# Optimization experiments

Measured on AMD Instinct MI355X. Metric: run time of the kernel, lower is better.

Reference implementation:

```python
import jax, jax.numpy as jnp
import numpy as np

NUM_HEADS = 4
LN_EPS = 1e-5


def _gcn_layer(src, dst, feats, skip_w, skip_b, msg_w, msg_b):
    # DGL GCNLayer: symmetric degree norm (from src rows), copy_u+sum aggregation,
    # msg linear + affine skip. No activation is applied in the original forward.
    n = feats.shape[0]
    deg = jax.ops.segment_sum(jnp.ones(src.shape, feats.dtype), src, num_segments=n)
    dinv = jnp.where(deg > 0, deg ** -0.5, jnp.zeros_like(deg))
    h = feats * dinv[:, None]                                  # [N, D]
    agg = jax.ops.segment_sum(h[src], dst, num_segments=n)     # scatter-sum over edges
    rst = agg * dinv[:, None]
    return rst @ msg_w.T + msg_b + feats @ skip_w.T + skip_b


def _layernorm(x, g, b):
    mu = jnp.mean(x, axis=-1, keepdims=True)
    var = jnp.mean((x - mu) ** 2, axis=-1, keepdims=True)
    return (x - mu) * jax.lax.rsqrt(var + LN_EPS) * g + b


def _cross_attention(x, seq, in_proj_w, in_proj_b, out_proj_w, out_proj_b, ln_g, ln_b):
    # Unbatched torch nn.MultiheadAttention(query=x [N,D], key=value=seq [S,D]).
    n, d = x.shape
    hd = d // NUM_HEADS
    wq, wk, wv = in_proj_w[:d], in_proj_w[d:2 * d], in_proj_w[2 * d:]
    bq, bk, bv = in_proj_b[:d], in_proj_b[d:2 * d], in_proj_b[2 * d:]
    q = (x @ wq.T + bq).reshape(n, NUM_HEADS, hd)
    k = (seq @ wk.T + bk).reshape(-1, NUM_HEADS, hd)
    v = (seq @ wv.T + bv).reshape(-1, NUM_HEADS, hd)
    scores = jnp.einsum('nhd,shd->hns', q, k) / jnp.sqrt(jnp.asarray(hd, x.dtype))
    attn = jax.nn.softmax(scores, axis=-1)
    o = jnp.einsum('hns,shd->nhd', attn, v).reshape(n, d)
    o = o @ out_proj_w.T + out_proj_b
    # dropout is identity in eval mode; residual + layernorm (num_cross_att == 1 path)
    return _layernorm(o + x, ln_g, ln_b)


def reference(x, seq_embeddings, src, dst, edge_label_index,
              skip_w0, skip_b0, msg_w0, msg_b0,
              skip_w1, skip_b1, msg_w1, msg_b1,
              in_proj_w, in_proj_b, out_proj_w, out_proj_b, ln_g, ln_b,
              weight1, weight2):
    x = _gcn_layer(src, dst, x, skip_w0, skip_b0, msg_w0, msg_b0)
    x = _gcn_layer(src, dst, x, skip_w1, skip_b1, msg_w1, msg_b1)
    x = _cross_attention(x, seq_embeddings, in_proj_w, in_proj_b,
                         out_proj_w, out_proj_b, ln_g, ln_b)
    # F.normalize: row-wise L2
    x = x / jnp.maximum(jnp.linalg.norm(x, axis=-1, keepdims=True), 1e-12)
    node_embedding = x
    p = jax.nn.relu(x @ weight1.T)                # dropout identity (eval)
    p = jax.nn.sigmoid(p @ weight2.T)[:, 0]       # [N]
    # dot edge decoding over last dim of size 1 -> elementwise product
    pred = p[edge_label_index[0]] * p[edge_label_index[1]]
    return pred, node_embedding


def setup_inputs() -> dict:
    key = jax.random.key(0)
    ks = jax.random.split(key, 20)
    N, E, S, D, K = 8192, 524288, 2048, 128, 100000
    s = 1.0 / np.sqrt(D)  # xavier-ish scale for weight matrices
    inp = {
        'x': jax.random.normal(ks[0], (N, D), jnp.float32),
        'seq_embeddings': jax.random.normal(ks[1], (S, D), jnp.float32),
        'src': jax.random.randint(ks[2], (E,), 0, N, jnp.int32),
        'dst': jax.random.randint(ks[3], (E,), 0, N, jnp.int32),
        'edge_label_index': jax.random.randint(ks[4], (2, K), 0, N, jnp.int32),
        'skip_w0': jax.random.normal(ks[5], (D, D), jnp.float32) * s,
        'skip_b0': jnp.zeros((D,), jnp.float32),
        'msg_w0': jax.random.normal(ks[6], (D, D), jnp.float32) * s,
        'msg_b0': jnp.zeros((D,), jnp.float32),
        'skip_w1': jax.random.normal(ks[7], (D, D), jnp.float32) * s,
        'skip_b1': jnp.zeros((D,), jnp.float32),
        'msg_w1': jax.random.normal(ks[8], (D, D), jnp.float32) * s,
        'msg_b1': jnp.zeros((D,), jnp.float32),
        'in_proj_w': jax.random.normal(ks[9], (3 * D, D), jnp.float32) * s,
        'in_proj_b': jnp.zeros((3 * D,), jnp.float32),
        'out_proj_w': jax.random.normal(ks[10], (D, D), jnp.float32) * s,
        'out_proj_b': jnp.zeros((D,), jnp.float32),
        'ln_g': jnp.ones((D,), jnp.float32),
        'ln_b': jnp.zeros((D,), jnp.float32),
        'weight1': jax.random.normal(ks[11], (D, D), jnp.float32) * s,
        'weight2': jax.random.normal(ks[12], (1, D), jnp.float32) * s,
    }
    return inp
```

## Files before the change

kernel.cpp:

```cpp
#include <hip/hip_runtime.h>
#include <math.h>

#define D 128
#define HB 128
#define FA_PS 88
#define SPLITS 8

typedef short bf16x4 __attribute__((ext_vector_type(4)));
typedef short bf16x8 __attribute__((ext_vector_type(8)));
typedef float f32x4 __attribute__((ext_vector_type(4)));

__device__ __forceinline__ float4 ld4(const float* p) { return *(const float4*)p; }

__device__ __forceinline__ short f2bf_r(float f) {
  return (short)((__float_as_uint(f) + 0x8000u) >> 16);
}
__device__ __forceinline__ float bf2f(short s) {
  return __uint_as_float(((unsigned)(unsigned short)s) << 16);
}
__device__ __forceinline__ unsigned pack_bf2(float a, float b) {
  unsigned ua = __float_as_uint(a) + 0x8000u;
  unsigned ub = __float_as_uint(b) + 0x8000u;
  return __builtin_amdgcn_perm(ub, ua, 0x07060302);
}

struct WSrc { const float* p[9]; };
__global__ __launch_bounds__(256) void prep0_kernel(WSrc ws, short* __restrict__ Wbf,
                                                    const float* __restrict__ x,
                                                    short* __restrict__ xbf,
                                                    int* __restrict__ MkhI) {
  int b = blockIdx.x, t = threadIdx.x;
  if (b == 0 && t < 4) MkhI[t] = 0;
  if (b < 144) {
    int m = b >> 4, blk = b & 15;
    int i = (blk * 256 + t) * 4;
    float4 v = ld4(ws.p[m] + i);
    bf16x4 o = {f2bf_r(v.x), f2bf_r(v.y), f2bf_r(v.z), f2bf_r(v.w)};
    *(bf16x4*)&Wbf[m * 16384 + i] = o;
  } else {
    int i = ((b - 144) * 256 + t) * 4;
    float4 v = ld4(x + i);
    bf16x4 o = {f2bf_r(v.x), f2bf_r(v.y), f2bf_r(v.z), f2bf_r(v.w)};
    *(bf16x4*)&xbf[i] = o;
  }
}

__global__ __launch_bounds__(256) void hist_kernel(
    const int* __restrict__ src, const int* __restrict__ dst,
    int* __restrict__ histd, int* __restrict__ hists, int E) {
  __shared__ int hd[8192];
  __shared__ int hs[8192];
  int t = threadIdx.x;
  for (int i = t; i < 8192; i += 256) { hd[i] = 0; hs[i] = 0; }
  __syncthreads();
  int per = E / HB;
  int b0 = blockIdx.x * per;
  for (int j = 0; j < per; j += 256) {
    int i = b0 + j + t;
    atomicAdd(&hd[dst[i]], 1);
    atomicAdd(&hs[src[i]], 1);
  }
  __syncthreads();
  for (int i = t; i < 8192; i += 256) {
    histd[blockIdx.x * 8192 + i] = hd[i];
    hists[blockIdx.x * 8192 + i] = hs[i];
  }
}

__global__ __launch_bounds__(256) void colsum_kernel(
    const int* __restrict__ histd, const int* __restrict__ hists,
    int* __restrict__ deg, float* __restrict__ dinv) {
  int v = blockIdx.x * 256 + threadIdx.x;
  int sd = 0, ss = 0;
  for (int b = 0; b < HB; ++b) { sd += histd[b * 8192 + v]; ss += hists[b * 8192 + v]; }
  deg[v] = sd;
  dinv[v] = ss > 0 ? rsqrtf((float)ss) : 0.f;
}

__global__ __launch_bounds__(1024) void scan8k_kernel(
    const int* __restrict__ deg, int* __restrict__ row_ptr, int N) {
  __shared__ int wtot[16];
  int t = threadIdx.x;
  int lane = t & 63, wv = t >> 6;
  int v0 = t * 8;
  int x[8]; int s = 0;
#pragma unroll
  for (int j = 0; j < 8; ++j) { x[j] = s; s += deg[v0 + j]; }
  int incl = s;
  for (int off = 1; off < 64; off <<= 1) {
    int y = __shfl_up(incl, off);
    if (lane >= off) incl += y;
  }
  if (lane == 63) wtot[wv] = incl;
  __syncthreads();
  if (t == 0) { int run = 0; for (int i = 0; i < 16; ++i) { int v = wtot[i]; wtot[i] = run; run += v; } }
  __syncthreads();
  int base = wtot[wv] + (incl - s);
#pragma unroll
  for (int j = 0; j < 8; ++j) row_ptr[v0 + j] = base + x[j];
  if (t == 1023) row_ptr[N] = base + s;
}

__global__ __launch_bounds__(256) void basegen_kernel(
    const int* __restrict__ histd, const int* __restrict__ row_ptr,
    int* __restrict__ base_arr) {
  int v = blockIdx.x * 256 + threadIdx.x;
  int run = row_ptr[v];
  for (int b = 0; b < HB; ++b) { base_arr[b * 8192 + v] = run; run += histd[b * 8192 + v]; }
}

__global__ __launch_bounds__(256) void scatter2_kernel(
    const int* __restrict__ src, const int* __restrict__ dst,
    const int* __restrict__ base_arr, int* __restrict__ csr_src, int E) {
  __shared__ int lh[8192];
  int t = threadIdx.x;
  for (int i = t; i < 8192; i += 256) lh[i] = 0;
  __syncthreads();
  int per = E / HB;
  int b0 = blockIdx.x * per;
  const int* __restrict__ bb = &base_arr[blockIdx.x * 8192];
  for (int j = 0; j < per; j += 256) {
    int i = b0 + j + t;
    int v = dst[i];
    int r = atomicAdd(&lh[v], 1);
    csr_src[bb[v] + r] = src[i];
  }
}

__global__ __launch_bounds__(128) void agg_kernel(
    const short* __restrict__ fbf, const float* __restrict__ dinv,
    const int* __restrict__ row_ptr, const int* __restrict__ csr_src,
    short* __restrict__ outbf) {
  __shared__ int idx[128];
  __shared__ float dv[128];
  __shared__ float red[8][128];
  int n = blockIdx.x, t = threadIdx.x;
  int grp = t >> 4, l16 = t & 15;
  int beg = row_ptr[n], end = row_ptr[n + 1];
  float a0[8] = {}, a1[8] = {}, a2[8] = {}, a3[8] = {};
  for (int c = beg; c < end; c += 128) {
    int j = c + t;
    if (j < end) { int s = csr_src[j]; idx[t] = s; dv[t] = dinv[s]; }
    __syncthreads();
    int cnt = min(128, end - c);
    int e = grp;
    for (; e + 24 < cnt; e += 32) {
      bf16x8 w0 = *(const bf16x8*)&fbf[(size_t)idx[e] * D + l16 * 8];
      bf16x8 w1 = *(const bf16x8*)&fbf[(size_t)idx[e + 8] * D + l16 * 8];
      bf16x8 w2 = *(const bf16x8*)&fbf[(size_t)idx[e + 16] * D + l16 * 8];
      bf16x8 w3 = *(const bf16x8*)&fbf[(size_t)idx[e + 24] * D + l16 * 8];
      float wt0 = dv[e], wt1 = dv[e + 8], wt2 = dv[e + 16], wt3 = dv[e + 24];
#pragma unroll
      for (int k = 0; k < 8; ++k) {
        a0[k] += bf2f(w0[k]) * wt0;
        a1[k] += bf2f(w1[k]) * wt1;
        a2[k] += bf2f(w2[k]) * wt2;
        a3[k] += bf2f(w3[k]) * wt3;
      }
    }
    for (; e < cnt; e += 8) {
      bf16x8 w0 = *(const bf16x8*)&fbf[(size_t)idx[e] * D + l16 * 8];
      float wt0 = dv[e];
#pragma unroll
      for (int k = 0; k < 8; ++k) a0[k] += bf2f(w0[k]) * wt0;
    }
    __syncthreads();
  }
#pragma unroll
  for (int k = 0; k < 8; ++k) a0[k] += a1[k] + a2[k] + a3[k];
  *(float4*)&red[grp][l16 * 8] = *(float4*)&a0[0];
  *(float4*)&red[grp][l16 * 8 + 4] = *(float4*)&a0[4];
  __syncthreads();
  if (t < 32) {
    int d0 = t * 4;
    float o[4] = {};
#pragma unroll
    for (int g = 0; g < 8; ++g) {
      o[0] += red[g][d0]; o[1] += red[g][d0 + 1];
      o[2] += red[g][d0 + 2]; o[3] += red[g][d0 + 3];
    }
    float w = dinv[n];
    bf16x4 ov = {f2bf_r(o[0] * w), f2bf_r(o[1] * w), f2bf_r(o[2] * w), f2bf_r(o[3] * w)};
    *(bf16x4*)&outbf[(size_t)n * D + d0] = ov;
  }
}

__device__ __forceinline__ void mfma_accum(const short* As, const short* __restrict__ W,
                                           int rt, int ch, int quad, int r16, f32x4* acc) {
#pragma unroll
  for (int ks = 0; ks < 4; ++ks) {
    bf16x8 af = *(bf16x8*)&As[(rt * 16 + r16) * 136 + ks * 32 + quad * 8];
#pragma unroll
    for (int nt = 0; nt < 4; ++nt) {
      bf16x8 bw = *(const bf16x8*)&W[(size_t)(ch * 64 + nt * 16 + r16) * D + ks * 32 + quad * 8];
      acc[nt] = __builtin_amdgcn_mfma_f32_16x16x32_bf16(af, bw, acc[nt], 0, 0, 0);
    }
  }
}

__device__ __forceinline__ void stage_A_f32(const float* __restrict__ A, int m0, short* As) {
  int row = threadIdx.x >> 3, seg = threadIdx.x & 7;
  const float* ap = &A[(size_t)(m0 + row) * D + seg * 16];
  float4 v0 = ld4(ap), v1 = ld4(ap + 4), v2 = ld4(ap + 8), v3 = ld4(ap + 12);
  bf16x8 w0 = {f2bf_r(v0.x), f2bf_r(v0.y), f2bf_r(v0.z), f2bf_r(v0.w),
               f2bf_r(v1.x), f2bf_r(v1.y), f2bf_r(v1.z), f2bf_r(v1.w)};
  bf16x8 w1 = {f2bf_r(v2.x), f2bf_r(v2.y), f2bf_r(v2.z), f2bf_r(v2.w),
               f2bf_r(v3.x), f2bf_r(v3.y), f2bf_r(v3.z), f2bf_r(v3.w)};
  *(bf16x8*)&As[row * 136 + seg * 16] = w0;
  *(bf16x8*)&As[row * 136 + seg * 16 + 8] = w1;
}

__device__ __forceinline__ void stage_A_bf16(const short* __restrict__ A, int m0, short* As) {
  int row = threadIdx.x >> 3, seg = threadIdx.x & 7;
  const short* ap = &A[(size_t)(m0 + row) * D + seg * 16];
  bf16x8 a0 = *(const bf16x8*)ap;
  bf16x8 a1 = *(const bf16x8*)(ap + 8);
  *(bf16x8*)&As[row * 136 + seg * 16] = a0;
  *(bf16x8*)&As[row * 136 + seg * 16 + 8] = a1;
}

__global__ __launch_bounds__(256) void gemm_gcn_kernel(
    const short* __restrict__ A1, const short* __restrict__ W1, const float* __restrict__ b1,
    const short* __restrict__ A2, const short* __restrict__ W2, const float* __restrict__ b2,
    short* __restrict__ Cbf, float* __restrict__ Cf) {
  __shared__ short As[32 * 136];
  const int t = threadIdx.x;
  const int m0 = blockIdx.x * 32;
  const int w = t >> 6, lane = t & 63, quad = lane >> 4, r16 = lane & 15;
  const int rt = w & 1, ch = w >> 1;
  f32x4 acc[4];
  f32x4 zz = {0.f, 0.f, 0.f, 0.f};
  acc[0] = zz; acc[1] = zz; acc[2] = zz; acc[3] = zz;
  stage_A_bf16(A1, m0, As);
  __syncthreads();
  mfma_accum(As, W1, rt, ch, quad, r16, acc);
  __syncthreads();
  stage_A_bf16(A2, m0, As);
  __syncthreads();
  mfma_accum(As, W2, rt, ch, quad, r16, acc);
#pragma unroll
  for (int nt = 0; nt < 4; ++nt) {
    int col = ch * 64 + nt * 16 + r16;
    float bias = b1[col] + b2[col];
#pragma unroll
    for (int g = 0; g < 4; ++g) {
      int row = m0 + rt * 16 + quad * 4 + g;
      float v = acc[nt][g] + bias;
      if (Cbf) Cbf[(size_t)row * D + col] = f2bf_r(v);
      if (Cf) Cf[(size_t)row * D + col] = v;
    }
  }
}

__global__ __launch_bounds__(256) void qkv_kernel(
    const float* __restrict__ B2, const float* __restrict__ seq,
    const short* __restrict__ Wq, const short* __restrict__ Wk, const short* __restrict__ Wv,
    const float* __restrict__ ipb,
    short* __restrict__ Qbf, float* __restrict__ qn,
    short* __restrict__ Kbf, int* __restrict__ MkhI,
    short* __restrict__ Vt, int N, int S) {
  __shared__ short As[32 * 136];
  __shared__ int lmax[4];
  const int t = threadIdx.x;
  const int b = blockIdx.x;
  const int w = t >> 6, lane = t & 63, quad = lane >> 4, r16 = lane & 15;
  const int rt = w & 1, ch = w >> 1;
  if (t < 4) lmax[t] = 0;
  f32x4 acc[4];
  f32x4 zz = {0.f, 0.f, 0.f, 0.f};
  acc[0] = zz; acc[1] = zz; acc[2] = zz; acc[3] = zz;
  const float SC = 0.25503473f;

  if (b < 256) {
    int m0 = b * 32;
    stage_A_f32(B2, m0, As);
    __syncthreads();
    mfma_accum(As, Wq, rt, ch, quad, r16, acc);
    float pq[4][2] = {};
#pragma unroll
    for (int nt = 0; nt < 4; ++nt) {
      int col = ch * 64 + nt * 16 + r16;
      float bias = ipb[col];
      int p = nt >> 1;
#pragma unroll
      for (int g = 0; g < 4; ++g) {
        int row = m0 + rt * 16 + quad * 4 + g;
        float vs = (acc[nt][g] + bias) * SC;
        Qbf[(size_t)row * D + col] = f2bf_r(vs);
        pq[g][p] += vs * vs;
      }
    }
#pragma unroll
    for (int mask = 1; mask < 16; mask <<= 1)
#pragma unroll
      for (int g = 0; g < 4; ++g) {
        pq[g][0] += __shfl_xor(pq[g][0], mask);
        pq[g][1] += __shfl_xor(pq[g][1], mask);
      }
    if (r16 == 0) {
#pragma unroll
      for (int g = 0; g < 4; ++g) {
        int row = m0 + rt * 16 + quad * 4 + g;
        qn[(ch * 2 + 0) * N + row] = sqrtf(pq[g][0]);
        qn[(ch * 2 + 1) * N + row] = sqrtf(pq[g][1]);
      }
    }
  } else if (b < 320) {
    int m0 = (b - 256) * 32;
    stage_A_f32(seq, m0, As);
    __syncthreads();
    mfma_accum(As, Wk, rt, ch, quad, r16, acc);
    float pk[4][2] = {};
#pragma unroll
    for (int nt = 0; nt < 4; ++nt) {
      int col = ch * 64 + nt * 16 + r16;
      float bias = ipb[128 + col];
      int p = nt >> 1;
#pragma unroll
      for (int g = 0; g < 4; ++g) {
        int key = m0 + rt * 16 + quad * 4 + g;
        float v = acc[nt][g] + bias;
        Kbf[(size_t)key * D + col] = f2bf_r(v);
        pk[g][p] += v * v;
      }
    }
#pragma unroll
    for (int mask = 1; mask < 16; mask <<= 1)
#pragma unroll
      for (int g = 0; g < 4; ++g) {
        pk[g][0] += __shfl_xor(pk[g][0], mask);
        pk[g][1] += __shfl_xor(pk[g][1], mask);
      }
    if (r16 == 0) {
#pragma unroll
      for (int g = 0; g < 4; ++g) {
        atomicMax(&lmax[ch * 2 + 0], __float_as_int(pk[g][0]));
        atomicMax(&lmax[ch * 2 + 1], __float_as_int(pk[g][1]));
      }
    }
    __syncthreads();
    if (t < 4) atomicMax(&MkhI[t], lmax[t]);
  } else {
    int m0 = (b - 320) * 32;
    stage_A_f32(seq, m0, As);
    __syncthreads();
    mfma_accum(As, Wv, rt, ch, quad, r16, acc);
#pragma unroll
    for (int nt = 0; nt < 4; ++nt) {
      int dim = ch * 64 + nt * 16 + r16;
      float bias = ipb[256 + dim];
#pragma unroll
      for (int g = 0; g < 4; ++g) {
        int s = m0 + rt * 16 + quad * 4 + g;
        int local = s & 63;
        int kp = (local & 15) * 4 + (local >> 4);
        int gcol = (s & ~63) + kp;
        Vt[(size_t)dim * S + gcol] = f2bf_r(acc[nt][g] + bias);
      }
    }
  }
}

__global__ __launch_bounds__(64, 8) void flash_kernel(
    const short* __restrict__ Qbf, const short* __restrict__ Kbf, const short* __restrict__ Vt,
    const float* __restrict__ qn, const int* __restrict__ MkhI,
    float* __restrict__ Osp, float* __restrict__ lbuf, int N, int S) {
  __shared__ short Ps[32 * FA_PS];
  const int lane = threadIdx.x;
  const int quad = lane >> 4, r16 = lane & 15;
  const int n0 = blockIdx.x * 32;
  const int h = blockIdx.y;
  const int sp = blockIdx.z;
  float* O = Osp + (size_t)sp * N * D;

  bf16x8 aq[2];
  aq[0] = *(const bf16x8*)&Qbf[(size_t)(n0 + r16) * D + h * 32 + quad * 8];
  aq[1] = *(const bf16x8*)&Qbf[(size_t)(n0 + 16 + r16) * D + h * 32 + quad * 8];

  float sqm = sqrtf(fmaxf(__int_as_float(MkhI[h]), 0.f));
  float msh[2][4];
#pragma unroll
  for (int rt = 0; rt < 2; ++rt)
#pragma unroll
    for (int g = 0; g < 4; ++g)
      msh[rt][g] = fminf(qn[h * N + n0 + rt * 16 + quad * 4 + g] * sqm, 57.7f);

  f32x4 o[2][2], lac[2];
  f32x4 zz = {0.f, 0.f, 0.f, 0.f};
  o[0][0] = zz; o[0][1] = zz; o[1][0] = zz; o[1][1] = zz;
  lac[0] = zz; lac[1] = zz;
  bf16x8 ones = {(short)0x3F80, (short)0x3F80, (short)0x3F80, (short)0x3F80,
                 (short)0x3F80, (short)0x3F80, (short)0x3F80, (short)0x3F80};

  const int span = S / SPLITS;
  const int c0 = sp * span;
  for (int c = c0; c < c0 + span; c += 64) {
    f32x4 s[2][4];
#pragma unroll
    for (int kt = 0; kt < 4; ++kt) {
      bf16x8 bk = *(const bf16x8*)&Kbf[(size_t)(c + kt * 16 + r16) * D + h * 32 + quad * 8];
      f32x4 z = {0.f, 0.f, 0.f, 0.f};
      s[0][kt] = __builtin_amdgcn_mfma_f32_16x16x32_bf16(aq[0], bk, z, 0, 0, 0);
      s[1][kt] = __builtin_amdgcn_mfma_f32_16x16x32_bf16(aq[1], bk, z, 0, 0, 0);
    }
#pragma unroll
    for (int rt = 0; rt < 2; ++rt)
#pragma unroll
      for (int g = 0; g < 4; ++g) {
        float m = msh[rt][g];
        float p0 = exp2f(s[rt][0][g] - m);
        float p1 = exp2f(s[rt][1][g] - m);
        float p2 = exp2f(s[rt][2][g] - m);
        float p3 = exp2f(s[rt][3][g] - m);
        uint2 uv = {pack_bf2(p0, p1), pack_bf2(p2, p3)};
        *(uint2*)&Ps[(rt * 16 + quad * 4 + g) * FA_PS + r16 * 4] = uv;
      }
    bf16x8 bv[2][2];
#pragma unroll
    for (int kc = 0; kc < 2; ++kc)
#pragma unroll
      for (int nt = 0; nt < 2; ++nt)
        bv[kc][nt] = *(const bf16x8*)&Vt[(size_t)(h * 32 + nt * 16 + r16) * S + c + kc * 32 + quad * 8];
#pragma unroll
    for (int rt = 0; rt < 2; ++rt)
#pragma unroll
      for (int kc = 0; kc < 2; ++kc) {
        bf16x8 ap = *(bf16x8*)&Ps[(rt * 16 + r16) * FA_PS + kc * 32 + quad * 8];
        lac[rt] = __builtin_amdgcn_mfma_f32_16x16x32_bf16(ap, ones, lac[rt], 0, 0, 0);
#pragma unroll
        for (int nt = 0; nt < 2; ++nt)
          o[rt][nt] = __builtin_amdgcn_mfma_f32_16x16x32_bf16(ap, bv[kc][nt], o[rt][nt], 0, 0, 0);
      }
  }
#pragma unroll
  for (int rt = 0; rt < 2; ++rt)
#pragma unroll
    for (int g = 0; g < 4; ++g) {
      int row = n0 + rt * 16 + quad * 4 + g;
#pragma unroll
      for (int nt = 0; nt < 2; ++nt)
        O[(size_t)row * D + h * 32 + nt * 16 + r16] = o[rt][nt][g];
      if (r16 == 0) lbuf[(sp * 4 + h) * N + row] = lac[rt][g];
    }
}

__global__ __launch_bounds__(256) void gemm_op_kernel(
    const float* __restrict__ Osp, const float* __restrict__ lbuf,
    const short* __restrict__ W, const float* __restrict__ bias,
    const float* __restrict__ Rres, const float* __restrict__ ln_g,
    const float* __restrict__ ln_b, float* __restrict__ emb, int N) {
  __shared__ short As[32 * 136];
  __shared__ float Cs[32 * 132];
  const int t = threadIdx.x;
  const int m0 = blockIdx.x * 32;
  const int w = t >> 6, lane = t & 63, quad = lane >> 4, r16 = lane & 15;
  const int rt = w & 1, ch = w >> 1;
  {
    int row = t >> 3, seg = t & 7;
    int grow = m0 + row;
    int hh = seg >> 1;
    float l = 0.f;
#pragma unroll
    for (int s = 0; s < SPLITS; ++s) l += lbuf[(s * 4 + hh) * N + grow];
    float inv = 1.f / l;
    const float* p = &Osp[(size_t)grow * D + seg * 16];
    size_t st = (size_t)N * D;
    float a16[16] = {};
#pragma unroll
    for (int s = 0; s < SPLITS; ++s) {
#pragma unroll
      for (int q = 0; q < 4; ++q) {
        float4 a = ld4(p + s * st + q * 4);
        a16[q * 4 + 0] += a.x; a16[q * 4 + 1] += a.y;
        a16[q * 4 + 2] += a.z; a16[q * 4 + 3] += a.w;
      }
    }
#pragma unroll
    for (int k = 0; k < 16; ++k) a16[k] *= inv;
    bf16x8 w0 = {f2bf_r(a16[0]), f2bf_r(a16[1]), f2bf_r(a16[2]), f2bf_r(a16[3]),
                 f2bf_r(a16[4]), f2bf_r(a16[5]), f2bf_r(a16[6]), f2bf_r(a16[7])};
    bf16x8 w1 = {f2bf_r(a16[8]), f2bf_r(a16[9]), f2bf_r(a16[10]), f2bf_r(a16[11]),
                 f2bf_r(a16[12]), f2bf_r(a16[13]), f2bf_r(a16[14]), f2bf_r(a16[15])};
    *(bf16x8*)&As[row * 136 + seg * 16] = w0;
    *(bf16x8*)&As[row * 136 + seg * 16 + 8] = w1;
  }
  __syncthreads();
  f32x4 acc[4];
  f32x4 zz = {0.f, 0.f, 0.f, 0.f};
  acc[0] = zz; acc[1] = zz; acc[2] = zz; acc[3] = zz;
  mfma_accum(As, W, rt, ch, quad, r16, acc);
#pragma unroll
  for (int nt = 0; nt < 4; ++nt) {
    int col = ch * 64 + nt * 16 + r16;
    float bs = bias[col];
#pragma unroll
    for (int g = 0; g < 4; ++g) {
      int lr = rt * 16 + quad * 4 + g;
      Cs[lr * 132 + col] = acc[nt][g] + bs + Rres[(size_t)(m0 + lr) * D + col];
    }
  }
  __syncthreads();
  {
    int row = t >> 3, seg = t & 7;
    float xv[16];
#pragma unroll
    for (int q = 0; q < 4; ++q) {
      f32x4 v = *(f32x4*)&Cs[row * 132 + seg * 16 + q * 4];
      xv[q * 4] = v[0]; xv[q * 4 + 1] = v[1]; xv[q * 4 + 2] = v[2]; xv[q * 4 + 3] = v[3];
    }
    float s = 0.f, sq = 0.f;
#pragma unroll
    for (int k = 0; k < 16; ++k) { s += xv[k]; sq += xv[k] * xv[k]; }
#pragma unroll
    for (int mask = 1; mask < 8; mask <<= 1) { s += __shfl_xor(s, mask); sq += __shfl_xor(sq, mask); }
    float mu = s * (1.f / 128.f);
    float var = fmaxf(sq * (1.f / 128.f) - mu * mu, 0.f);
    float rs = rsqrtf(var + 1e-5f);
    float yv[16], nn = 0.f;
#pragma unroll
    for (int q = 0; q < 4; ++q) {
      float4 gg = ld4(&ln_g[seg * 16 + q * 4]);
      float4 bb = ld4(&ln_b[seg * 16 + q * 4]);
      float y0 = (xv[q * 4] - mu) * rs * gg.x + bb.x;
      float y1 = (xv[q * 4 + 1] - mu) * rs * gg.y + bb.y;
      float y2 = (xv[q * 4 + 2] - mu) * rs * gg.z + bb.z;
      float y3 = (xv[q * 4 + 3] - mu) * rs * gg.w + bb.w;
      yv[q * 4] = y0; yv[q * 4 + 1] = y1; yv[q * 4 + 2] = y2; yv[q * 4 + 3] = y3;
      nn += y0 * y0 + y1 * y1 + y2 * y2 + y3 * y3;
    }
#pragma unroll
    for (int mask = 1; mask < 8; mask <<= 1) nn += __shfl_xor(nn, mask);
    float inv = 1.f / fmaxf(sqrtf(nn), 1e-12f);
#pragma unroll
    for (int q = 0; q < 4; ++q) {
      float4 ov = {yv[q * 4] * inv, yv[q * 4 + 1] * inv, yv[q * 4 + 2] * inv, yv[q * 4 + 3] * inv};
      *(float4*)&emb[(size_t)(m0 + row) * D + seg * 16 + q * 4] = ov;
    }
  }
}

__global__ __launch_bounds__(256) void gemm_mlp_kernel(
    const float* __restrict__ emb, const short* __restrict__ W,
    const float* __restrict__ w2, float* __restrict__ pbuf) {
  __shared__ short As[32 * 136];
  __shared__ float part[32][2];
  const int t = threadIdx.x;
  const int m0 = blockIdx.x * 32;
  const int w = t >> 6, lane = t & 63, quad = lane >> 4, r16 = lane & 15;
  const int rt = w & 1, ch = w >> 1;
  stage_A_f32(emb, m0, As);
  __syncthreads();
  f32x4 acc[4];
  f32x4 zz = {0.f, 0.f, 0.f, 0.f};
  acc[0] = zz; acc[1] = zz; acc[2] = zz; acc[3] = zz;
  mfma_accum(As, W, rt, ch, quad, r16, acc);
  float pg[4] = {};
#pragma unroll
  for (int nt = 0; nt < 4; ++nt) {
    float wv = w2[ch * 64 + nt * 16 + r16];
#pragma unroll
    for (int g = 0; g < 4; ++g) pg[g] += fmaxf(acc[nt][g], 0.f) * wv;
  }
#pragma unroll
  for (int mask = 1; mask < 16; mask <<= 1)
#pragma unroll
    for (int g = 0; g < 4; ++g) pg[g] += __shfl_xor(pg[g], mask);
  if (r16 == 0) {
#pragma unroll
    for (int g = 0; g < 4; ++g) part[rt * 16 + quad * 4 + g][ch] = pg[g];
  }
  __syncthreads();
  if (t < 32) {
    float sv = part[t][0] + part[t][1];
    pbuf[m0 + t] = 1.f / (1.f + __expf(-sv));
  }
}

__global__ void pred_kernel(const float* __restrict__ p, const int* __restrict__ eli,
                            float* __restrict__ out, int K) {
  int i = blockIdx.x * blockDim.x + threadIdx.x;
  if (i < K) out[i] = p[eli[i]] * p[eli[K + i]];
}

extern "C" void kernel_launch(void* const* d_in, const int* in_sizes, int n_in,
                              void* d_out, int out_size, void* d_ws, size_t ws_size,
                              hipStream_t stream) {
  const float* x       = (const float*)d_in[0];
  const float* seq     = (const float*)d_in[1];
  const int* src       = (const int*)d_in[2];
  const int* dst       = (const int*)d_in[3];
  const int* eli       = (const int*)d_in[4];
  const float* skip_w0 = (const float*)d_in[5];
  const float* skip_b0 = (const float*)d_in[6];
  const float* msg_w0  = (const float*)d_in[7];
  const float* msg_b0  = (const float*)d_in[8];
  const float* skip_w1 = (const float*)d_in[9];
  const float* skip_b1 = (const float*)d_in[10];
  const float* msg_w1  = (const float*)d_in[11];
  const float* msg_b1  = (const float*)d_in[12];
  const float* ipw     = (const float*)d_in[13];
  const float* ipb     = (const float*)d_in[14];
  const float* opw     = (const float*)d_in[15];
  const float* opb     = (const float*)d_in[16];
  const float* ln_g    = (const float*)d_in[17];
  const float* ln_b    = (const float*)d_in[18];
  const float* w1      = (const float*)d_in[19];
  const float* w2      = (const float*)d_in[20];

  const int N  = in_sizes[0] / D;
  const int S  = in_sizes[1] / D;
  const int E  = in_sizes[2];
  const int Kp = in_sizes[4] / 2;

  float* ws    = (float*)d_ws;
  float* B2    = ws;
  float* Osp   = B2 + (size_t)N * D;
  short* xbf   = (short*)(Osp + (size_t)SPLITS * N * D);
  short* Abf   = xbf + (size_t)N * D;
  short* B1bf  = Abf + (size_t)N * D;
  short* Qbf   = B1bf + (size_t)N * D;
  short* Kbf   = Qbf + (size_t)N * D;
  short* Vt    = Kbf + (size_t)S * D;
  short* Wbf   = Vt + (size_t)D * S;
  float* qn    = (float*)(Wbf + 9 * 16384);
  float* lbuf  = qn + 4 * (size_t)N;
  float* dinv  = lbuf + 4 * (size_t)SPLITS * N;
  float* pbuf  = dinv + N;
  int*   MkhI  = (int*)(pbuf + N);
  int*   deg   = MkhI + 4;
  int* row_ptr = deg + N;
  int* csr_src = row_ptr + (N + 1);
  int* histd   = csr_src + E;
  int* hists   = histd + HB * 8192;
  int* base_arr= hists + HB * 8192;

  float* pred_out = (float*)d_out;
  float* emb_out  = pred_out + Kp;

  const short* w_skip0 = Wbf + 0 * 16384;
  const short* w_msg0  = Wbf + 1 * 16384;
  const short* w_skip1 = Wbf + 2 * 16384;
  const short* w_msg1  = Wbf + 3 * 16384;
  const short* w_q     = Wbf + 4 * 16384;
  const short* w_k     = Wbf + 5 * 16384;
  const short* w_v     = Wbf + 6 * 16384;
  const short* w_op    = Wbf + 7 * 16384;
  const short* w_m1    = Wbf + 8 * 16384;

  WSrc wsrc;
  wsrc.p[0] = skip_w0; wsrc.p[1] = msg_w0; wsrc.p[2] = skip_w1; wsrc.p[3] = msg_w1;
  wsrc.p[4] = ipw; wsrc.p[5] = ipw + D * D; wsrc.p[6] = ipw + 2 * D * D;
  wsrc.p[7] = opw; wsrc.p[8] = w1;
  prep0_kernel<<<144 + (N * D / 1024), 256, 0, stream>>>(wsrc, (short*)Wbf, x, xbf, MkhI);

  hist_kernel<<<HB, 256, 0, stream>>>(src, dst, histd, hists, E);
  colsum_kernel<<<N / 256, 256, 0, stream>>>(histd, hists, deg, dinv);
  scan8k_kernel<<<1, 1024, 0, stream>>>(deg, row_ptr, N);
  basegen_kernel<<<N / 256, 256, 0, stream>>>(histd, row_ptr, base_arr);
  scatter2_kernel<<<HB, 256, 0, stream>>>(src, dst, base_arr, csr_src, E);

  agg_kernel<<<N, 128, 0, stream>>>(xbf, dinv, row_ptr, csr_src, Abf);
  gemm_gcn_kernel<<<N / 32, 256, 0, stream>>>(Abf, w_msg0, msg_b0, xbf, w_skip0, skip_b0, B1bf, nullptr);
  agg_kernel<<<N, 128, 0, stream>>>(B1bf, dinv, row_ptr, csr_src, Abf);
  gemm_gcn_kernel<<<N / 32, 256, 0, stream>>>(Abf, w_msg1, msg_b1, B1bf, w_skip1, skip_b1, nullptr, B2);

  qkv_kernel<<<N / 32 + 2 * (S / 32), 256, 0, stream>>>(
      B2, seq, w_q, w_k, w_v, ipb, Qbf, qn, Kbf, MkhI, Vt, N, S);

  dim3 fgrid(N / 32, 4, SPLITS);
  flash_kernel<<<fgrid, 64, 0, stream>>>(Qbf, Kbf, Vt, qn, MkhI, Osp, lbuf, N, S);
  gemm_op_kernel<<<N / 32, 256, 0, stream>>>(Osp, lbuf, w_op, opb, B2, ln_g, ln_b, emb_out, N);

  gemm_mlp_kernel<<<N / 32, 256, 0, stream>>>(emb_out, w_m1, w2, pbuf);
  pred_kernel<<<(Kp + 255) / 256, 256, 0, stream>>>(pbuf, eli, pred_out, Kp);
}
```

Baseline: 285.4 us.

## Store Q and K head-major and halve flash-attention key splits

Q and K are now written in a head-major layout ([head][row][32]), so each flash block reads contiguous 64-byte rows for its head instead of strided slices of 256-byte rows. The number of key splits drops from 8 to 4, and the launch-bounds occupancy hint drops from 8 to 4 accordingly. This gives fewer partial outputs for gemm_op to combine and less Osp traffic, at the cost of fewer flash blocks and a longer serial loop per block.

```diff
diff --git a/kernel.cpp b/kernel.cpp
--- a/kernel.cpp
+++ b/kernel.cpp
@@ -4,7 +4,7 @@
 #define D 128
 #define HB 128
 #define FA_PS 88
-#define SPLITS 8
+#define SPLITS 4
 
 typedef short bf16x4 __attribute__((ext_vector_type(4)));
 typedef short bf16x8 __attribute__((ext_vector_type(8)));
@@ -256,8 +256,8 @@
     const float* __restrict__ B2, const float* __restrict__ seq,
     const short* __restrict__ Wq, const short* __restrict__ Wk, const short* __restrict__ Wv,
     const float* __restrict__ ipb,
-    short* __restrict__ Qbf, float* __restrict__ qn,
-    short* __restrict__ Kbf, int* __restrict__ MkhI,
+    short* __restrict__ Qh, float* __restrict__ qn,
+    short* __restrict__ Kh, int* __restrict__ MkhI,
     short* __restrict__ Vt, int N, int S) {
   __shared__ short As[32 * 136];
   __shared__ int lmax[4];
@@ -280,13 +280,14 @@
 #pragma unroll
     for (int nt = 0; nt < 4; ++nt) {
       int col = ch * 64 + nt * 16 + r16;
+      int hq = col >> 5, dq = col & 31;
       float bias = ipb[col];
       int p = nt >> 1;
 #pragma unroll
       for (int g = 0; g < 4; ++g) {
         int row = m0 + rt * 16 + quad * 4 + g;
         float vs = (acc[nt][g] + bias) * SC;
-        Qbf[(size_t)row * D + col] = f2bf_r(vs);
+        Qh[((size_t)hq * N + row) * 32 + dq] = f2bf_r(vs);
         pq[g][p] += vs * vs;
       }
     }
@@ -314,13 +315,14 @@
 #pragma unroll
     for (int nt = 0; nt < 4; ++nt) {
       int col = ch * 64 + nt * 16 + r16;
+      int hk = col >> 5, dk = col & 31;
       float bias = ipb[128 + col];
       int p = nt >> 1;
 #pragma unroll
       for (int g = 0; g < 4; ++g) {
         int key = m0 + rt * 16 + quad * 4 + g;
         float v = acc[nt][g] + bias;
-        Kbf[(size_t)key * D + col] = f2bf_r(v);
+        Kh[((size_t)hk * S + key) * 32 + dk] = f2bf_r(v);
         pk[g][p] += v * v;
       }
     }
@@ -361,8 +363,8 @@
   }
 }
 
-__global__ __launch_bounds__(64, 8) void flash_kernel(
-    const short* __restrict__ Qbf, const short* __restrict__ Kbf, const short* __restrict__ Vt,
+__global__ __launch_bounds__(64, 4) void flash_kernel(
+    const short* __restrict__ Qh, const short* __restrict__ Kh, const short* __restrict__ Vt,
     const float* __restrict__ qn, const int* __restrict__ MkhI,
     float* __restrict__ Osp, float* __restrict__ lbuf, int N, int S) {
   __shared__ short Ps[32 * FA_PS];
@@ -372,10 +374,12 @@
   const int h = blockIdx.y;
   const int sp = blockIdx.z;
   float* O = Osp + (size_t)sp * N * D;
+  const short* Kb = Kh + (size_t)h * S * 32;
+  const short* Qb = Qh + (size_t)h * N * 32;
 
   bf16x8 aq[2];
-  aq[0] = *(const bf16x8*)&Qbf[(size_t)(n0 + r16) * D + h * 32 + quad * 8];
-  aq[1] = *(const bf16x8*)&Qbf[(size_t)(n0 + 16 + r16) * D + h * 32 + quad * 8];
+  aq[0] = *(const bf16x8*)&Qb[(size_t)(n0 + r16) * 32 + quad * 8];
+  aq[1] = *(const bf16x8*)&Qb[(size_t)(n0 + 16 + r16) * 32 + quad * 8];
 
   float sqm = sqrtf(fmaxf(__int_as_float(MkhI[h]), 0.f));
   float msh[2][4];
@@ -398,7 +402,7 @@
     f32x4 s[2][4];
 #pragma unroll
     for (int kt = 0; kt < 4; ++kt) {
-      bf16x8 bk = *(const bf16x8*)&Kbf[(size_t)(c + kt * 16 + r16) * D + h * 32 + quad * 8];
+      bf16x8 bk = *(const bf16x8*)&Kb[(size_t)(c + kt * 16 + r16) * 32 + quad * 8];
       f32x4 z = {0.f, 0.f, 0.f, 0.f};
       s[0][kt] = __builtin_amdgcn_mfma_f32_16x16x32_bf16(aq[0], bk, z, 0, 0, 0);
       s[1][kt] = __builtin_amdgcn_mfma_f32_16x16x32_bf16(aq[1], bk, z, 0, 0, 0);
@@ -618,9 +622,9 @@
   short* xbf   = (short*)(Osp + (size_t)SPLITS * N * D);
   short* Abf   = xbf + (size_t)N * D;
   short* B1bf  = Abf + (size_t)N * D;
-  short* Qbf   = B1bf + (size_t)N * D;
-  short* Kbf   = Qbf + (size_t)N * D;
-  short* Vt    = Kbf + (size_t)S * D;
+  short* Qh    = B1bf + (size_t)N * D;
+  short* Kh    = Qh + (size_t)N * D;
+  short* Vt    = Kh + (size_t)S * D;
   short* Wbf   = Vt + (size_t)D * S;
   float* qn    = (float*)(Wbf + 9 * 16384);
   float* lbuf  = qn + 4 * (size_t)N;
@@ -665,10 +669,10 @@
   gemm_gcn_kernel<<<N / 32, 256, 0, stream>>>(Abf, w_msg1, msg_b1, B1bf, w_skip1, skip_b1, nullptr, B2);
 
   qkv_kernel<<<N / 32 + 2 * (S / 32), 256, 0, stream>>>(
-      B2, seq, w_q, w_k, w_v, ipb, Qbf, qn, Kbf, MkhI, Vt, N, S);
+      B2, seq, w_q, w_k, w_v, ipb, Qh, qn, Kh, MkhI, Vt, N, S);
 
   dim3 fgrid(N / 32, 4, SPLITS);
-  flash_kernel<<<fgrid, 64, 0, stream>>>(Qbf, Kbf, Vt, qn, MkhI, Osp, lbuf, N, S);
+  flash_kernel<<<fgrid, 64, 0, stream>>>(Qh, Kh, Vt, qn, MkhI, Osp, lbuf, N, S);
   gemm_op_kernel<<<N / 32, 256, 0, stream>>>(Osp, lbuf, w_op, opb, B2, ln_g, ln_b, emb_out, N);
 
   gemm_mlp_kernel<<<N / 32, 256, 0, stream>>>(emb_out, w_m1, w2, pbuf);
```

New measurement: 234.7 us. 17.8% less time.
